# Kernel tuning notes

Measured on AMD Instinct MI355X. Metric: run time of the kernel, lower is better.

The kernel has to match this reference:

```python
import jax, jax.numpy as jnp
import numpy as np
from jax import lax

B, N, G, K, D = 32, 32768, 64, 32, 384
EPS = 1e-5


def _fps(xyz, npoint):
    # Farthest point sampling; deterministic start at index 0 (original uses randint).
    b, n, _ = xyz.shape
    def step(carry, _):
        distance, farthest = carry
        centroid = jnp.take_along_axis(xyz, farthest[:, None, None], axis=1)  # (B,1,3)
        dist = jnp.sum((xyz - centroid) ** 2, axis=-1)                        # (B,N)
        distance = jnp.minimum(distance, dist)
        new_far = jnp.argmax(distance, axis=-1)
        return (distance, new_far), farthest
    init = (jnp.full((b, n), 1e10, xyz.dtype), jnp.zeros((b,), jnp.int32))
    _, cents = lax.scan(step, init, None, length=npoint)  # (npoint, B)
    return cents.T  # (B, npoint)


def _bn(h, g, bta, m, v):
    # inference-mode BatchNorm over channel (last) dim
    return (h - m) * (g * lax.rsqrt(v + EPS)) + bta


def setup_inputs() -> dict:
    key = jax.random.key(0)
    ks = jax.random.split(key, 5)
    xyz = jax.random.normal(ks[0], (B, N, 3), jnp.float32)
    features = jax.random.normal(ks[1], (B, N, 3), jnp.float32)
    w1 = jax.random.normal(ks[2], (64, 6), jnp.float32) * 0.1
    w2 = jax.random.normal(ks[3], (128, 64), jnp.float32) * 0.1
    w3 = jax.random.normal(ks[4], (D, 128), jnp.float32) * 0.1
    def bn(c):
        return jnp.ones((c,), jnp.float32), jnp.zeros((c,), jnp.float32), jnp.zeros((c,), jnp.float32), jnp.ones((c,), jnp.float32)
    g1, b1, m1, v1 = bn(64)
    g2, b2, m2, v2 = bn(128)
    g3, b3, m3, v3 = bn(D)
    return dict(xyz=xyz, features=features, w1=w1, g1=g1, b1=b1, m1=m1, v1=v1,
                w2=w2, g2=g2, b2=b2, m2=m2, v2=v2, w3=w3, g3=g3, b3=b3, m3=m3, v3=v3)


def reference(xyz, features, w1, g1, b1, m1, v1, w2, g2, b2, m2, v2, w3, g3, b3, m3, v3):
    fps_idx = _fps(xyz, G)                                           # (B,G)
    center = jnp.take_along_axis(xyz, fps_idx[:, :, None], axis=1)   # (B,G,3)
    # KNN via squared distances (same ordering as torch.cdist euclidean)
    xn2 = jnp.sum(xyz * xyz, axis=-1)                                # (B,N)
    cn2 = jnp.sum(center * center, axis=-1)                          # (B,G)
    d2 = cn2[:, :, None] + xn2[:, None, :] - 2.0 * jnp.einsum('bgc,bnc->bgn', center, xyz)
    _, knn_idx = lax.top_k(-d2, K)                                   # (B,G,K)
    gx = jax.vmap(lambda x, i: x[i])(xyz, knn_idx)                   # (B,G,K,3)
    gf = jax.vmap(lambda f, i: f[i])(features, knn_idx)              # (B,G,K,3)
    h = jnp.concatenate([gx - center[:, :, None, :], gf], axis=-1)   # (B,G,K,6)
    h = jax.nn.relu(_bn(jnp.einsum('bgkc,oc->bgko', h, w1), g1, b1, m1, v1))
    h = jax.nn.relu(_bn(jnp.einsum('bgkc,oc->bgko', h, w2), g2, b2, m2, v2))
    h = _bn(jnp.einsum('bgkc,oc->bgko', h, w3), g3, b3, m3, v3)      # (B,G,K,D)
    patch = jnp.max(h, axis=2)                                       # (B,G,D) adaptive max pool
    return center, patch
```

## Files before the change

### kernel.cpp

```cpp
#include <hip/hip_runtime.h>
#include <hip/hip_bf16.h>

#define BB 32
#define NN 32768
#define GG 64
#define KK 32
#define DD 384
#define EPSF 1e-5f
#define FPS_NBLK 8
#define FPS_SL   (NN/FPS_NBLK)

typedef __attribute__((ext_vector_type(8))) short short8;
typedef __attribute__((ext_vector_type(4))) float f32x4;

__device__ __forceinline__ float rn_add(float a, float b){ return __fadd_rn(a,b); }
__device__ __forceinline__ float rn_sub(float a, float b){ return __fsub_rn(a,b); }
__device__ __forceinline__ float rn_mul(float a, float b){ return __fmul_rn(a,b); }

__device__ __forceinline__ unsigned fkey(float d){
  unsigned u = __float_as_uint(d);
  return (u & 0x80000000u) ? ~u : (u | 0x80000000u);
}

__device__ __forceinline__ unsigned short f2bf(float f){
  unsigned u = __float_as_uint(f);
  unsigned r = (u + 0x7FFFu + ((u >> 16) & 1u)) >> 16;
  return (unsigned short)r;
}

#define REP16(X) X(0) X(1) X(2) X(3) X(4) X(5) X(6) X(7) \
                 X(8) X(9) X(10) X(11) X(12) X(13) X(14) X(15)

__device__ float g_center[BB*GG*3];
__device__ int   g_knn[BB*GG*KK];
__device__ float g_w1t[6*64];
__device__ float g_b1[64];
__device__ float g_b2[128];
__device__ float g_b3[384];
__device__ __align__(16) unsigned short g_w2f[8*2*64*8];
__device__ __align__(16) unsigned short g_w3f[24*4*64*8];
__device__ float g_X[BB*NN];
__device__ float g_Y[BB*NN];
__device__ float g_Z[BB*NN];
__device__ float g_N2[BB*NN];
__device__ unsigned long long g_part[BB*FPS_NBLK*GG];

__global__ __launch_bounds__(256) void k_soa(const float* __restrict__ xyz){
  int tid = blockIdx.x * blockDim.x + threadIdx.x;
  int b = tid >> 15;
  int p = tid & (NN - 1);
  const float* s = xyz + (size_t)b*NN*3 + (size_t)p*3;
  float x = s[0], y = s[1], z = s[2];
  g_X[tid] = x;
  g_Y[tid] = y;
  g_Z[tid] = z;
  g_N2[tid] = rn_add(rn_add(rn_mul(x,x), rn_mul(y,y)), rn_mul(z,z));
}

__global__ __launch_bounds__(256) void k_zero(void){
  int tid = blockIdx.x * blockDim.x + threadIdx.x;
  if (tid < BB*FPS_NBLK*GG) g_part[tid] = 0ull;
}

__global__ void k_prep(const float* __restrict__ w1, const float* __restrict__ g1, const float* __restrict__ b1, const float* __restrict__ m1, const float* __restrict__ v1,
                       const float* __restrict__ w2, const float* __restrict__ g2, const float* __restrict__ b2, const float* __restrict__ m2, const float* __restrict__ v2,
                       const float* __restrict__ w3, const float* __restrict__ g3, const float* __restrict__ b3, const float* __restrict__ m3, const float* __restrict__ v3){
  int tid = blockIdx.x * blockDim.x + threadIdx.x;
  int nt  = gridDim.x * blockDim.x;
  for (int e = tid; e < 64*6; e += nt){
    int c = e >> 6, o = e & 63;
    float s = g1[o] * rsqrtf(v1[o] + EPSF);
    g_w1t[e] = w1[o*6 + c] * s;
  }
  for (int o = tid; o < 64; o += nt){
    float s = g1[o] * rsqrtf(v1[o] + EPSF);
    g_b1[o] = b1[o] - m1[o]*s;
  }
  for (int o = tid; o < 128; o += nt){
    float s = g2[o] * rsqrtf(v2[o] + EPSF);
    g_b2[o] = b2[o] - m2[o]*s;
  }
  for (int o = tid; o < 384; o += nt){
    float s = g3[o] * rsqrtf(v3[o] + EPSF);
    g_b3[o] = b3[o] - m3[o]*s;
  }
  for (int idx = tid; idx < 8192; idx += nt){
    int e  = idx & 7;
    int l  = (idx >> 3) & 63;
    int kt = (idx >> 9) & 1;
    int ct = idx >> 10;
    int j  = ct*16 + (l & 15);
    int k  = kt*32 + ((l >> 4) << 3) + e;
    float s = g2[j] * rsqrtf(v2[j] + EPSF);
    g_w2f[idx] = f2bf(w2[j*64 + k] * s);
  }
  for (int idx = tid; idx < 49152; idx += nt){
    int e  = idx & 7;
    int l  = (idx >> 3) & 63;
    int kt = (idx >> 9) & 3;
    int ct = idx >> 11;
    int j  = ct*16 + (l & 15);
    int k  = kt*32 + ((l >> 4) << 3) + e;
    float s = g3[j] * rsqrtf(v3[j] + EPSF);
    g_w3f[idx] = f2bf(w3[j*128 + k] * s);
  }
}

__global__ __launch_bounds__(256)
void k_fps(float* __restrict__ outCenter){
  const int blk = blockIdx.x;
  const int b   = blk >> 3;
  const int sub = blk & 7;
  const int t   = threadIdx.x;
  const int wv  = t >> 6, ln = t & 63;
  const int base = sub * FPS_SL;
  const float* Xb = g_X + (size_t)b*NN;
  const float* Yb = g_Y + (size_t)b*NN;
  const float* Zb = g_Z + (size_t)b*NN;

  __shared__ float sx[FPS_SL], sy[FPS_SL], szz[FPS_SL];
  __shared__ unsigned long long skey[4];
  __shared__ int s_far;

  #pragma unroll
  for (int i = 0; i < 16; ++i){
    int p = (i << 8) + t;
    sx[p]  = Xb[base + p];
    sy[p]  = Yb[base + p];
    szz[p] = Zb[base + p];
  }
  __syncthreads();

#define DD_DECL(i) float dd##i = 1e10f;
  REP16(DD_DECL)
#undef DD_DECL

  int far = 0;
  for (int it = 0; ; ++it){
    if (sub == 0 && t == 0){
      float cx = Xb[far], cy = Yb[far], cz = Zb[far];
      float* cw = g_center  + (size_t)(b*GG + it)*3;
      float* co = outCenter + (size_t)(b*GG + it)*3;
      cw[0] = cx; cw[1] = cy; cw[2] = cz;
      co[0] = cx; co[1] = cy; co[2] = cz;
    }
    if (it == GG - 1) break;

    float cx = Xb[far], cy = Yb[far], cz = Zb[far];
    unsigned long long bk = 0ull;
#define DD_UPD(i) { \
    int p = (i << 8) + t; \
    float dx = rn_sub(sx[p], cx); \
    float dy = rn_sub(sy[p], cy); \
    float dz = rn_sub(szz[p], cz); \
    float s_ = rn_add(rn_add(rn_mul(dx,dx), rn_mul(dy,dy)), rn_mul(dz,dz)); \
    float d_ = fminf(dd##i, s_); \
    dd##i = d_; \
    unsigned long long k_ = ((unsigned long long)fkey(d_) << 32) \
                          | (unsigned)(0xFFFFFFFFu - (unsigned)(base + p)); \
    if (k_ > bk) bk = k_; }
    REP16(DD_UPD)
#undef DD_UPD

    #pragma unroll
    for (int off = 32; off >= 1; off >>= 1){
      unsigned long long o = (unsigned long long)__shfl_xor((long long)bk, off);
      if (o > bk) bk = o;
    }
    if (ln == 0) skey[wv] = bk;
    __syncthreads();
    if (wv == 0){
      unsigned long long m = (ln < 4) ? skey[ln] : 0ull;
      #pragma unroll
      for (int off = 1; off <= 2; off <<= 1){
        unsigned long long o = (unsigned long long)__shfl_xor((long long)m, off);
        if (o > m) m = o;
      }
      if (ln == 0)
        atomicExch(&g_part[(((b << 3) + sub) << 6) + it], m);
      unsigned long long k = 0ull;
      if (ln < 8){
        unsigned long long* p = &g_part[(((b << 3) + ln) << 6) + it];
        do { k = atomicAdd(p, 0ull); } while (k == 0ull);
      }
      #pragma unroll
      for (int off = 1; off <= 4; off <<= 1){
        unsigned long long o = (unsigned long long)__shfl_xor((long long)k, off);
        if (o > k) k = o;
      }
      if (ln == 0) s_far = (int)(0xFFFFFFFFu - (unsigned)(k & 0xFFFFFFFFu));
    }
    __syncthreads();
    far = s_far;
  }
}

__global__ __launch_bounds__(256) void k_knn(void){
  const int bg = blockIdx.x;
  const int b  = bg >> 6;
  const int t  = threadIdx.x;
  const int w  = t >> 6;
  const int ln = t & 63;
  const float4* X4 = (const float4*)(g_X  + (size_t)b*NN);
  const float4* Y4 = (const float4*)(g_Y  + (size_t)b*NN);
  const float4* Z4 = (const float4*)(g_Z  + (size_t)b*NN);
  const float4* N4 = (const float4*)(g_N2 + (size_t)b*NN);

  __shared__ unsigned sE[64];
  __shared__ unsigned long long s_cand[512];
  __shared__ int s_cnt;

  const float* cp = g_center + (size_t)bg*3;
  float cx = cp[0], cy = cp[1], cz = cp[2];
  float cn2 = rn_add(rn_add(rn_mul(cx,cx), rn_mul(cy,cy)), rn_mul(cz,cz));

  float e0 = INFINITY, e1 = INFINITY;
  #pragma unroll 2
  for (int s = 0; s < 32; ++s){
    int q = (s << 8) + t;
    float4 x = X4[q], y = Y4[q], z = Z4[q], n = N4[q];
    #define D2C(c) { \
      float e = rn_add(rn_add(rn_mul(cx,x.c), rn_mul(cy,y.c)), rn_mul(cz,z.c)); \
      float d = rn_sub(rn_add(cn2, n.c), rn_add(e,e)); \
      if (d < e1){ if (d < e0){ e1 = e0; e0 = d; } else e1 = d; } }
    D2C(x) D2C(y) D2C(z) D2C(w)
    #undef D2C
  }

  {
    unsigned v = fkey(e1);
    #pragma unroll
    for (int k = 2; k <= 64; k <<= 1){
      #pragma unroll
      for (int j = k >> 1; j > 0; j >>= 1){
        unsigned o = (unsigned)__shfl_xor((int)v, j);
        bool keepmin = (((ln & k) == 0) == ((ln & j) == 0));
        unsigned mn = o < v ? o : v;
        unsigned mx = o < v ? v : o;
        v = keepmin ? mn : mx;
      }
    }
    if (ln < 16) sE[w*16 + ln] = v;
  }
  if (t == 0) s_cnt = 0;
  __syncthreads();

  unsigned T;
  {
    unsigned v = sE[ln];
    #pragma unroll
    for (int k = 2; k <= 64; k <<= 1){
      #pragma unroll
      for (int j = k >> 1; j > 0; j >>= 1){
        unsigned o = (unsigned)__shfl_xor((int)v, j);
        bool keepmin = (((ln & k) == 0) == ((ln & j) == 0));
        unsigned mn = o < v ? o : v;
        unsigned mx = o < v ? v : o;
        v = keepmin ? mn : mx;
      }
    }
    T = (unsigned)__shfl((int)v, 15);
  }

  #pragma unroll 2
  for (int s = 0; s < 32; ++s){
    int q = (s << 8) + t;
    float4 x = X4[q], y = Y4[q], z = Z4[q], n = N4[q];
    #define COLC(c, kk) { \
      float e = rn_add(rn_add(rn_mul(cx,x.c), rn_mul(cy,y.c)), rn_mul(cz,z.c)); \
      float d = rn_sub(rn_add(cn2, n.c), rn_add(e,e)); \
      unsigned fk = fkey(d); \
      if (fk <= T){ \
        int p = atomicAdd(&s_cnt, 1); \
        if (p < 512) \
          s_cand[p] = ((unsigned long long)fk << 32) | (unsigned)((q<<2)+kk); } }
    COLC(x,0) COLC(y,1) COLC(z,2) COLC(w,3)
    #undef COLC
  }
  __syncthreads();

  if (w == 0){
    int C = s_cnt; if (C > 512) C = 512;
    int* kout = g_knn + (size_t)bg*KK;
    if (C <= 64){
      unsigned long long kk = (ln < C) ? s_cand[ln] : ~0ull;
      #pragma unroll
      for (int k = 2; k <= 64; k <<= 1){
        #pragma unroll
        for (int j = k >> 1; j > 0; j >>= 1){
          unsigned long long o = (unsigned long long)__shfl_xor((long long)kk, j);
          bool keepmin = (((ln & k) == 0) == ((ln & j) == 0));
          unsigned long long mn = o < kk ? o : kk;
          unsigned long long mx = o < kk ? kk : o;
          kk = keepmin ? mn : mx;
        }
      }
      if (ln < KK) kout[ln] = (int)(kk & 0xffffffffu);
    } else {
      unsigned long long md[8];
      #pragma unroll
      for (int j = 0; j < 8; ++j){
        int e = ln + (j << 6);
        md[j] = (e < C) ? s_cand[e] : ~0ull;
      }
      for (int r = 0; r < KK; ++r){
        unsigned long long bk = md[0];
        #pragma unroll
        for (int j = 1; j < 8; ++j) if (md[j] < bk) bk = md[j];
        #pragma unroll
        for (int off = 32; off >= 1; off >>= 1){
          unsigned long long o = (unsigned long long)__shfl_xor((long long)bk, off);
          if (o < bk) bk = o;
        }
        #pragma unroll
        for (int j = 0; j < 8; ++j) if (md[j] == bk) md[j] = ~0ull;
        if (ln == 0) kout[r] = (int)(bk & 0xffffffffu);
      }
    }
  }
}

__global__ __launch_bounds__(256) void k_mlp(const float* __restrict__ xyz,
                                             const float* __restrict__ feat,
                                             float* __restrict__ outPatch){
  const int bg = blockIdx.x;
  const int b  = bg >> 6;
  const int t  = threadIdx.x;
  const int w  = t >> 6;
  const int ln = t & 63;
  const float* xb = xyz  + (size_t)b*NN*3;
  const float* fb = feat + (size_t)b*NN*3;

  __shared__ float h0[KK][8];
  __shared__ __align__(16) unsigned short h1b[KK][72];
  __shared__ __align__(16) unsigned short h2b[KK][136];

  if (t < KK){
    int idx = g_knn[(size_t)bg*KK + t] & (NN - 1);
    const float* cp = g_center + (size_t)bg*3;
    h0[t][0] = rn_sub(xb[idx*3+0], cp[0]);
    h0[t][1] = rn_sub(xb[idx*3+1], cp[1]);
    h0[t][2] = rn_sub(xb[idx*3+2], cp[2]);
    h0[t][3] = fb[idx*3+0];
    h0[t][4] = fb[idx*3+1];
    h0[t][5] = fb[idx*3+2];
  }
  __syncthreads();

  {
    int p = t >> 3, ob = (t & 7) * 8;
    float acc[8];
    #pragma unroll
    for (int j = 0; j < 8; ++j) acc[j] = g_b1[ob + j];
    #pragma unroll
    for (int c = 0; c < 6; ++c){
      float a = h0[p][c];
      const float4* wr = (const float4*)(g_w1t + c*64 + ob);
      float4 wa = wr[0], wb = wr[1];
      acc[0] = fmaf(a, wa.x, acc[0]); acc[1] = fmaf(a, wa.y, acc[1]);
      acc[2] = fmaf(a, wa.z, acc[2]); acc[3] = fmaf(a, wa.w, acc[3]);
      acc[4] = fmaf(a, wb.x, acc[4]); acc[5] = fmaf(a, wb.y, acc[5]);
      acc[6] = fmaf(a, wb.z, acc[6]); acc[7] = fmaf(a, wb.w, acc[7]);
    }
    short8 v;
    #pragma unroll
    for (int j = 0; j < 8; ++j) v[j] = (short)f2bf(fmaxf(acc[j], 0.f));
    *reinterpret_cast<short8*>(&h1b[p][ob]) = v;
  }
  __syncthreads();

  {
    f32x4 a00 = {0,0,0,0}, a01 = {0,0,0,0}, a10 = {0,0,0,0}, a11 = {0,0,0,0};
    const int g8 = (ln >> 4) << 3;
    #pragma unroll
    for (int kk = 0; kk < 2; ++kk){
      short8 A0 = *reinterpret_cast<const short8*>(&h1b[(ln & 15)][kk*32 + g8]);
      short8 A1 = *reinterpret_cast<const short8*>(&h1b[16 + (ln & 15)][kk*32 + g8]);
      short8 B0 = *reinterpret_cast<const short8*>(&g_w2f[(((2*w+0)*2 + kk)*64 + ln)*8]);
      short8 B1 = *reinterpret_cast<const short8*>(&g_w2f[(((2*w+1)*2 + kk)*64 + ln)*8]);
      a00 = __builtin_amdgcn_mfma_f32_16x16x32_bf16(A0, B0, a00, 0, 0, 0);
      a01 = __builtin_amdgcn_mfma_f32_16x16x32_bf16(A1, B0, a01, 0, 0, 0);
      a10 = __builtin_amdgcn_mfma_f32_16x16x32_bf16(A0, B1, a10, 0, 0, 0);
      a11 = __builtin_amdgcn_mfma_f32_16x16x32_bf16(A1, B1, a11, 0, 0, 0);
    }
    int col0 = (2*w)*16 + (ln & 15);
    int col1 = col0 + 16;
    float bz0 = g_b2[col0], bz1 = g_b2[col1];
    int r0 = (ln >> 4) << 2;
    #pragma unroll
    for (int r = 0; r < 4; ++r){
      h2b[r0 + r][col0]      = f2bf(fmaxf(a00[r] + bz0, 0.f));
      h2b[16 + r0 + r][col0] = f2bf(fmaxf(a01[r] + bz0, 0.f));
      h2b[r0 + r][col1]      = f2bf(fmaxf(a10[r] + bz1, 0.f));
      h2b[16 + r0 + r][col1] = f2bf(fmaxf(a11[r] + bz1, 0.f));
    }
  }
  __syncthreads();

  {
    f32x4 acc3[6][2];
    #pragma unroll
    for (int ci = 0; ci < 6; ++ci){
      acc3[ci][0] = (f32x4){0,0,0,0};
      acc3[ci][1] = (f32x4){0,0,0,0};
    }
    const int g8 = (ln >> 4) << 3;
    #pragma unroll
    for (int kk = 0; kk < 4; ++kk){
      short8 A0 = *reinterpret_cast<const short8*>(&h2b[(ln & 15)][kk*32 + g8]);
      short8 A1 = *reinterpret_cast<const short8*>(&h2b[16 + (ln & 15)][kk*32 + g8]);
      #pragma unroll
      for (int ci = 0; ci < 6; ++ci){
        int ct = w*6 + ci;
        short8 B = *reinterpret_cast<const short8*>(&g_w3f[((ct*4 + kk)*64 + ln)*8]);
        acc3[ci][0] = __builtin_amdgcn_mfma_f32_16x16x32_bf16(A0, B, acc3[ci][0], 0, 0, 0);
        acc3[ci][1] = __builtin_amdgcn_mfma_f32_16x16x32_bf16(A1, B, acc3[ci][1], 0, 0, 0);
      }
    }
    #pragma unroll
    for (int ci = 0; ci < 6; ++ci){
      float m = acc3[ci][0][0];
      #pragma unroll
      for (int r = 1; r < 4; ++r) m = fmaxf(m, acc3[ci][0][r]);
      #pragma unroll
      for (int r = 0; r < 4; ++r) m = fmaxf(m, acc3[ci][1][r]);
      m = fmaxf(m, __shfl_xor(m, 16));
      m = fmaxf(m, __shfl_xor(m, 32));
      if (ln < 16){
        int col = (w*6 + ci)*16 + ln;
        outPatch[(size_t)bg*DD + col] = m + g_b3[col];
      }
    }
  }
}

extern "C" void kernel_launch(void* const* d_in, const int* in_sizes, int n_in,
                              void* d_out, int out_size, void* d_ws, size_t ws_size,
                              hipStream_t stream){
  (void)in_sizes; (void)n_in; (void)out_size; (void)d_ws; (void)ws_size;
  const float* xyz  = (const float*)d_in[0];
  const float* feat = (const float*)d_in[1];
  const float* w1 = (const float*)d_in[2];
  const float* g1 = (const float*)d_in[3];
  const float* b1 = (const float*)d_in[4];
  const float* m1 = (const float*)d_in[5];
  const float* v1 = (const float*)d_in[6];
  const float* w2 = (const float*)d_in[7];
  const float* g2 = (const float*)d_in[8];
  const float* b2 = (const float*)d_in[9];
  const float* m2 = (const float*)d_in[10];
  const float* v2 = (const float*)d_in[11];
  const float* w3 = (const float*)d_in[12];
  const float* g3 = (const float*)d_in[13];
  const float* b3 = (const float*)d_in[14];
  const float* m3 = (const float*)d_in[15];
  const float* v3 = (const float*)d_in[16];
  float* out = (float*)d_out;

  k_prep<<<64, 256, 0, stream>>>(w1,g1,b1,m1,v1, w2,g2,b2,m2,v2, w3,g3,b3,m3,v3);
  k_soa<<<(BB*NN)/256, 256, 0, stream>>>(xyz);
  k_zero<<<64, 256, 0, stream>>>();
  k_fps<<<BB*FPS_NBLK, 256, 0, stream>>>(out);
  k_knn<<<BB*GG, 256, 0, stream>>>();
  k_mlp<<<BB*GG, 256, 0, stream>>>(xyz, feat, out + (size_t)BB*GG*3);
}
```

Before: 300.9 us.

## Process eight KNN centers per block and merge setup kernels into one

```diff
diff --git a/kernel.cpp b/kernel.cpp
--- a/kernel.cpp
+++ b/kernel.cpp
@@ -45,28 +45,19 @@
 __device__ float g_N2[BB*NN];
 __device__ unsigned long long g_part[BB*FPS_NBLK*GG];
 
-__global__ __launch_bounds__(256) void k_soa(const float* __restrict__ xyz){
-  int tid = blockIdx.x * blockDim.x + threadIdx.x;
-  int b = tid >> 15;
-  int p = tid & (NN - 1);
-  const float* s = xyz + (size_t)b*NN*3 + (size_t)p*3;
-  float x = s[0], y = s[1], z = s[2];
-  g_X[tid] = x;
-  g_Y[tid] = y;
-  g_Z[tid] = z;
-  g_N2[tid] = rn_add(rn_add(rn_mul(x,x), rn_mul(y,y)), rn_mul(z,z));
-}
-
-__global__ __launch_bounds__(256) void k_zero(void){
-  int tid = blockIdx.x * blockDim.x + threadIdx.x;
-  if (tid < BB*FPS_NBLK*GG) g_part[tid] = 0ull;
-}
-
-__global__ void k_prep(const float* __restrict__ w1, const float* __restrict__ g1, const float* __restrict__ b1, const float* __restrict__ m1, const float* __restrict__ v1,
+__global__ __launch_bounds__(256) void k_pre(const float* __restrict__ xyz,
+                       const float* __restrict__ w1, const float* __restrict__ g1, const float* __restrict__ b1, const float* __restrict__ m1, const float* __restrict__ v1,
                        const float* __restrict__ w2, const float* __restrict__ g2, const float* __restrict__ b2, const float* __restrict__ m2, const float* __restrict__ v2,
                        const float* __restrict__ w3, const float* __restrict__ g3, const float* __restrict__ b3, const float* __restrict__ m3, const float* __restrict__ v3){
   int tid = blockIdx.x * blockDim.x + threadIdx.x;
   int nt  = gridDim.x * blockDim.x;
+  {
+    const float* s = xyz + (size_t)tid*3;
+    float x = s[0], y = s[1], z = s[2];
+    g_X[tid] = x; g_Y[tid] = y; g_Z[tid] = z;
+    g_N2[tid] = rn_add(rn_add(rn_mul(x,x), rn_mul(y,y)), rn_mul(z,z));
+  }
+  if (tid < BB*FPS_NBLK*GG) g_part[tid] = 0ull;
   for (int e = tid; e < 64*6; e += nt){
     int c = e >> 6, o = e & 63;
     float s = g1[o] * rsqrtf(v1[o] + EPSF);
@@ -89,20 +80,20 @@
     int l  = (idx >> 3) & 63;
     int kt = (idx >> 9) & 1;
     int ct = idx >> 10;
-    int j  = ct*16 + (l & 15);
+    int jj = ct*16 + (l & 15);
     int k  = kt*32 + ((l >> 4) << 3) + e;
-    float s = g2[j] * rsqrtf(v2[j] + EPSF);
-    g_w2f[idx] = f2bf(w2[j*64 + k] * s);
+    float s = g2[jj] * rsqrtf(v2[jj] + EPSF);
+    g_w2f[idx] = f2bf(w2[jj*64 + k] * s);
   }
   for (int idx = tid; idx < 49152; idx += nt){
     int e  = idx & 7;
     int l  = (idx >> 3) & 63;
     int kt = (idx >> 9) & 3;
     int ct = idx >> 11;
-    int j  = ct*16 + (l & 15);
+    int jj = ct*16 + (l & 15);
     int k  = kt*32 + ((l >> 4) << 3) + e;
-    float s = g3[j] * rsqrtf(v3[j] + EPSF);
-    g_w3f[idx] = f2bf(w3[j*128 + k] * s);
+    float s = g3[jj] * rsqrtf(v3[jj] + EPSF);
+    g_w3f[idx] = f2bf(w3[jj*128 + k] * s);
   }
 }
 
@@ -196,8 +187,9 @@
 }
 
 __global__ __launch_bounds__(256) void k_knn(void){
-  const int bg = blockIdx.x;
-  const int b  = bg >> 6;
+  const int j  = blockIdx.x;
+  const int b  = (j & 7) + (((j >> 3) >> 3) << 3);
+  const int g0 = ((j >> 3) & 7) << 3;
   const int t  = threadIdx.x;
   const int w  = t >> 6;
   const int ln = t & 63;
@@ -206,90 +198,121 @@
   const float4* Z4 = (const float4*)(g_Z  + (size_t)b*NN);
   const float4* N4 = (const float4*)(g_N2 + (size_t)b*NN);
 
-  __shared__ unsigned sE[64];
-  __shared__ unsigned long long s_cand[512];
-  __shared__ int s_cnt;
-
-  const float* cp = g_center + (size_t)bg*3;
-  float cx = cp[0], cy = cp[1], cz = cp[2];
-  float cn2 = rn_add(rn_add(rn_mul(cx,cx), rn_mul(cy,cy)), rn_mul(cz,cz));
-
-  float e0 = INFINITY, e1 = INFINITY;
+  __shared__ float sC[4][8];
+  __shared__ unsigned sE[8][64];
+  __shared__ unsigned sTk[8];
+  __shared__ unsigned long long cand[8][512];
+  __shared__ int cnt[8];
+
+  if (t < 8){
+    const float* cp = g_center + (size_t)(b*GG + g0 + t)*3;
+    float x = cp[0], y = cp[1], z = cp[2];
+    sC[0][t] = x; sC[1][t] = y; sC[2][t] = z;
+    sC[3][t] = rn_add(rn_add(rn_mul(x,x), rn_mul(y,y)), rn_mul(z,z));
+    cnt[t] = 0;
+  }
+  __syncthreads();
+
+  float cx[8], cy[8], cz[8], cn[8];
+  #pragma unroll
+  for (int c = 0; c < 8; ++c){
+    cx[c] = sC[0][c]; cy[c] = sC[1][c]; cz[c] = sC[2][c]; cn[c] = sC[3][c];
+  }
+
+  float e0[8], e1[8];
+  #pragma unroll
+  for (int c = 0; c < 8; ++c){ e0[c] = INFINITY; e1[c] = INFINITY; }
   #pragma unroll 2
   for (int s = 0; s < 32; ++s){
     int q = (s << 8) + t;
     float4 x = X4[q], y = Y4[q], z = Z4[q], n = N4[q];
-    #define D2C(c) { \
-      float e = rn_add(rn_add(rn_mul(cx,x.c), rn_mul(cy,y.c)), rn_mul(cz,z.c)); \
-      float d = rn_sub(rn_add(cn2, n.c), rn_add(e,e)); \
-      if (d < e1){ if (d < e0){ e1 = e0; e0 = d; } else e1 = d; } }
-    D2C(x) D2C(y) D2C(z) D2C(w)
-    #undef D2C
-  }
-
-  {
-    unsigned v = fkey(e1);
+    #pragma unroll
+    for (int c = 0; c < 8; ++c){
+      #define D2C(cc) { \
+        float e = rn_add(rn_add(rn_mul(cx[c],x.cc), rn_mul(cy[c],y.cc)), rn_mul(cz[c],z.cc)); \
+        float d = rn_sub(rn_add(cn[c], n.cc), rn_add(e,e)); \
+        float nm2 = fminf(e1[c], fmaxf(e0[c], d)); \
+        e0[c] = fminf(e0[c], d); \
+        e1[c] = nm2; }
+      D2C(x) D2C(y) D2C(z) D2C(w)
+      #undef D2C
+    }
+  }
+
+  #pragma unroll
+  for (int c = 0; c < 8; ++c){
+    unsigned v = fkey(e1[c]);
     #pragma unroll
     for (int k = 2; k <= 64; k <<= 1){
       #pragma unroll
-      for (int j = k >> 1; j > 0; j >>= 1){
-        unsigned o = (unsigned)__shfl_xor((int)v, j);
-        bool keepmin = (((ln & k) == 0) == ((ln & j) == 0));
+      for (int jj = k >> 1; jj > 0; jj >>= 1){
+        unsigned o = (unsigned)__shfl_xor((int)v, jj);
+        bool keepmin = (((ln & k) == 0) == ((ln & jj) == 0));
         unsigned mn = o < v ? o : v;
         unsigned mx = o < v ? v : o;
         v = keepmin ? mn : mx;
       }
     }
-    if (ln < 16) sE[w*16 + ln] = v;
-  }
-  if (t == 0) s_cnt = 0;
-  __syncthreads();
-
-  unsigned T;
-  {
-    unsigned v = sE[ln];
+    if (ln < 16) sE[c][w*16 + ln] = v;
+  }
+  __syncthreads();
+
+  #pragma unroll
+  for (int cc = 0; cc < 2; ++cc){
+    int c = 2*w + cc;
+    unsigned v = sE[c][ln];
     #pragma unroll
     for (int k = 2; k <= 64; k <<= 1){
       #pragma unroll
-      for (int j = k >> 1; j > 0; j >>= 1){
-        unsigned o = (unsigned)__shfl_xor((int)v, j);
-        bool keepmin = (((ln & k) == 0) == ((ln & j) == 0));
+      for (int jj = k >> 1; jj > 0; jj >>= 1){
+        unsigned o = (unsigned)__shfl_xor((int)v, jj);
+        bool keepmin = (((ln & k) == 0) == ((ln & jj) == 0));
         unsigned mn = o < v ? o : v;
         unsigned mx = o < v ? v : o;
         v = keepmin ? mn : mx;
       }
     }
-    T = (unsigned)__shfl((int)v, 15);
-  }
+    if (ln == 15) sTk[c] = v;
+  }
+  __syncthreads();
+
+  unsigned Tr[8];
+  #pragma unroll
+  for (int c = 0; c < 8; ++c) Tr[c] = sTk[c];
 
   #pragma unroll 2
   for (int s = 0; s < 32; ++s){
     int q = (s << 8) + t;
     float4 x = X4[q], y = Y4[q], z = Z4[q], n = N4[q];
-    #define COLC(c, kk) { \
-      float e = rn_add(rn_add(rn_mul(cx,x.c), rn_mul(cy,y.c)), rn_mul(cz,z.c)); \
-      float d = rn_sub(rn_add(cn2, n.c), rn_add(e,e)); \
-      unsigned fk = fkey(d); \
-      if (fk <= T){ \
-        int p = atomicAdd(&s_cnt, 1); \
-        if (p < 512) \
-          s_cand[p] = ((unsigned long long)fk << 32) | (unsigned)((q<<2)+kk); } }
-    COLC(x,0) COLC(y,1) COLC(z,2) COLC(w,3)
-    #undef COLC
-  }
-  __syncthreads();
-
-  if (w == 0){
-    int C = s_cnt; if (C > 512) C = 512;
-    int* kout = g_knn + (size_t)bg*KK;
+    #pragma unroll
+    for (int c = 0; c < 8; ++c){
+      #define COLC(cc, kk) { \
+        float e = rn_add(rn_add(rn_mul(cx[c],x.cc), rn_mul(cy[c],y.cc)), rn_mul(cz[c],z.cc)); \
+        float d = rn_sub(rn_add(cn[c], n.cc), rn_add(e,e)); \
+        unsigned fk = fkey(d); \
+        if (fk <= Tr[c]){ \
+          int p = atomicAdd(&cnt[c], 1); \
+          if (p < 512) \
+            cand[c][p] = ((unsigned long long)fk << 32) | (unsigned)((q<<2)+kk); } }
+      COLC(x,0) COLC(y,1) COLC(z,2) COLC(w,3)
+      #undef COLC
+    }
+  }
+  __syncthreads();
+
+  #pragma unroll
+  for (int cc = 0; cc < 2; ++cc){
+    int c = 2*w + cc;
+    int C = cnt[c]; if (C > 512) C = 512;
+    int* kout = g_knn + (size_t)(b*GG + g0 + c)*KK;
     if (C <= 64){
-      unsigned long long kk = (ln < C) ? s_cand[ln] : ~0ull;
+      unsigned long long kk = (ln < C) ? cand[c][ln] : ~0ull;
       #pragma unroll
       for (int k = 2; k <= 64; k <<= 1){
         #pragma unroll
-        for (int j = k >> 1; j > 0; j >>= 1){
-          unsigned long long o = (unsigned long long)__shfl_xor((long long)kk, j);
-          bool keepmin = (((ln & k) == 0) == ((ln & j) == 0));
+        for (int jj = k >> 1; jj > 0; jj >>= 1){
+          unsigned long long o = (unsigned long long)__shfl_xor((long long)kk, jj);
+          bool keepmin = (((ln & k) == 0) == ((ln & jj) == 0));
           unsigned long long mn = o < kk ? o : kk;
           unsigned long long mx = o < kk ? kk : o;
           kk = keepmin ? mn : mx;
@@ -299,21 +322,21 @@
     } else {
       unsigned long long md[8];
       #pragma unroll
-      for (int j = 0; j < 8; ++j){
-        int e = ln + (j << 6);
-        md[j] = (e < C) ? s_cand[e] : ~0ull;
+      for (int jj = 0; jj < 8; ++jj){
+        int e = ln + (jj << 6);
+        md[jj] = (e < C) ? cand[c][e] : ~0ull;
       }
       for (int r = 0; r < KK; ++r){
         unsigned long long bk = md[0];
         #pragma unroll
-        for (int j = 1; j < 8; ++j) if (md[j] < bk) bk = md[j];
+        for (int jj = 1; jj < 8; ++jj) if (md[jj] < bk) bk = md[jj];
         #pragma unroll
         for (int off = 32; off >= 1; off >>= 1){
           unsigned long long o = (unsigned long long)__shfl_xor((long long)bk, off);
           if (o < bk) bk = o;
         }
         #pragma unroll
-        for (int j = 0; j < 8; ++j) if (md[j] == bk) md[j] = ~0ull;
+        for (int jj = 0; jj < 8; ++jj) if (md[jj] == bk) md[jj] = ~0ull;
         if (ln == 0) kout[r] = (int)(bk & 0xffffffffu);
       }
     }
@@ -457,10 +480,9 @@
   const float* v3 = (const float*)d_in[16];
   float* out = (float*)d_out;
 
-  k_prep<<<64, 256, 0, stream>>>(w1,g1,b1,m1,v1, w2,g2,b2,m2,v2, w3,g3,b3,m3,v3);
-  k_soa<<<(BB*NN)/256, 256, 0, stream>>>(xyz);
-  k_zero<<<64, 256, 0, stream>>>();
+  k_pre<<<(BB*NN)/256, 256, 0, stream>>>(xyz,
+      w1,g1,b1,m1,v1, w2,g2,b2,m2,v2, w3,g3,b3,m3,v3);
   k_fps<<<BB*FPS_NBLK, 256, 0, stream>>>(out);
-  k_knn<<<BB*GG, 256, 0, stream>>>();
+  k_knn<<<256, 256, 0, stream>>>();
   k_mlp<<<BB*GG, 256, 0, stream>>>(xyz, feat, out + (size_t)BB*GG*3);
 }
```

New measurement: 326.6 us. +8.6%, slower.
